# Kernel optimization log

Hardware: AMD Instinct MI355X
Metric: run time of the kernel (lower is better)

Reference implementation:

```python
import jax, jax.numpy as jnp
import numpy as np

N_NODES = 100000
N_EDGES = 3200000
DIMS = [3, 64, 64, 64, 128, 1024, 512, 256, 2]  # per GCNemb.__init__


def setup_inputs() -> dict:
    key = jax.random.key(0)
    ks = jax.random.split(key, 2 + 2 * 8)
    x = jax.random.normal(ks[0], (N_NODES, DIMS[0]), dtype=jnp.float32)
    edge_index = jax.random.randint(ks[1], (2, N_EDGES), 0, N_NODES, dtype=jnp.int64)
    inp = {"x": x, "edge_index": edge_index}
    for i in range(8):
        scale = 1.0 / np.sqrt(DIMS[i])
        inp[f"W{i}"] = jax.random.normal(ks[2 + 2 * i], (DIMS[i], DIMS[i + 1]), dtype=jnp.float32) * scale
        inp[f"b{i}"] = jnp.zeros((DIMS[i + 1],), dtype=jnp.float32)
    return inp


def _gcn_norm(edge_index, n):
    # PyG GCNConv default: add self-loops, symmetric normalization.
    loop = jnp.arange(n, dtype=edge_index.dtype)
    row = jnp.concatenate([edge_index[0], loop])  # source
    col = jnp.concatenate([edge_index[1], loop])  # target
    deg = jax.ops.segment_sum(jnp.ones_like(col, dtype=jnp.float32), col, num_segments=n)
    dinv = jnp.where(deg > 0, jax.lax.rsqrt(deg), 0.0)
    norm = dinv[row] * dinv[col]  # [E+N]
    return row, col, norm


def _gcn_conv(x, W, b, row, col, norm, n):
    h = x @ W  # [N, out]
    agg = jax.ops.segment_sum(h[row] * norm[:, None], col, num_segments=n)
    return agg + b


def reference(x, edge_index, W0, b0, W1, b1, W2, b2, W3, b3, W4, b4, W5, b5, W6, b6, W7, b7):
    n = x.shape[0]
    row, col, norm = _gcn_norm(edge_index, n)
    Ws = [W0, W1, W2, W3, W4, W5, W6, W7]
    bs = [b0, b1, b2, b3, b4, b5, b6, b7]
    for i in range(7):
        x = jax.nn.relu(_gcn_conv(x, Ws[i], bs[i], row, col, norm, n))
    return _gcn_conv(x, Ws[7], bs[7], row, col, norm, n)
```

## Files before the change

### kernel.cpp

```cpp
#include <hip/hip_runtime.h>
#include <hip/hip_bf16.h>
#include <cstdint>
#include <cstddef>


#define TPB 256

typedef short short8 __attribute__((ext_vector_type(8)));
typedef float f32x4 __attribute__((ext_vector_type(4)));

__device__ __forceinline__ float b2f(unsigned short u) {
    union { unsigned int i; float f; } c; c.i = ((unsigned int)u) << 16; return c.f;
}
__device__ __forceinline__ unsigned short f2b(float f) {
    __hip_bfloat16 h = __float2bfloat16(f);
    union { __hip_bfloat16 h; unsigned short u; } c; c.h = h; return c.u;
}

__device__ __forceinline__ void async_copy16(void* lds, const void* g) {
    __builtin_amdgcn_global_load_lds(
        (const __attribute__((address_space(1))) void*)g,
        (__attribute__((address_space(3))) void*)lds,
        16, 0, 0);
}


__global__ void count_deg_kernel(const int* __restrict__ col, int* __restrict__ deg,
                                 int E, int n) {
    int e = blockIdx.x * blockDim.x + threadIdx.x;
    if (e < E) {
        int c = col[e];
        if ((unsigned)c < (unsigned)n) atomicAdd(&deg[c], 1);
    }
}

__global__ void dinv_kernel(const int* __restrict__ deg, float* __restrict__ dinv, int n) {
    int i = blockIdx.x * blockDim.x + threadIdx.x;
    if (i < n) dinv[i] = 1.0f / sqrtf((float)(deg[i] + 1));
}

__global__ void scan_kernel(const int* __restrict__ deg, int* __restrict__ rowptr,
                            int* __restrict__ cursor, int n) {
    __shared__ int sums[1024];
    int tid = threadIdx.x;
    int chunk = (n + 1023) >> 10;
    int lo = tid * chunk;
    int hi = lo + chunk; if (hi > n) hi = n;
    int s = 0;
    for (int i = lo; i < hi; i++) s += deg[i];
    sums[tid] = s;
    __syncthreads();
    for (int off = 1; off < 1024; off <<= 1) {
        int v = (tid >= off) ? sums[tid - off] : 0;
        __syncthreads();
        sums[tid] += v;
        __syncthreads();
    }
    int run = (tid == 0) ? 0 : sums[tid - 1];
    for (int i = lo; i < hi; i++) {
        rowptr[i] = run; cursor[i] = run;
        run += deg[i];
    }
    if (tid == 1023) rowptr[n] = sums[1023];
}

__global__ void fill_csr_kernel(const int* __restrict__ row, const int* __restrict__ col,
                                const float* __restrict__ dinv,
                                int* __restrict__ cursor, int2* __restrict__ es,
                                int E, int n) {
    int e = blockIdx.x * blockDim.x + threadIdx.x;
    if (e < E) {
        int c = col[e];
        if ((unsigned)c < (unsigned)n) {
            int r = row[e];
            int pos = atomicAdd(&cursor[c], 1);
            if ((unsigned)pos < (unsigned)E) {
                es[pos] = make_int2(r, __float_as_int(dinv[r]));
            }
        }
    }
}

__global__ void convert_wt_kernel(const float* __restrict__ W, unsigned short* __restrict__ Wt,
                                  int K, int M) {
    int idx = blockIdx.x * blockDim.x + threadIdx.x;
    if (idx < K * M) {
        int k = idx / M, m = idx % M;
        Wt[(size_t)m * K + k] = f2b(W[idx]);
    }
}


template <int VEC> struct Pack;
template <> struct Pack<1> { using T = unsigned short; };
template <> struct Pack<2> { using T = unsigned int; };
template <> struct Pack<4> { using T = uint2; };

template <int VEC>
__global__ __launch_bounds__(TPB) void agg_win_kernel(
        const unsigned short* __restrict__ x, unsigned short* __restrict__ out,
        const int* __restrict__ rowptr, const int2* __restrict__ es,
        const float* __restrict__ dinv, const float* __restrict__ bias,
        int n, int d, int wb, int relu) {
    using P = typename Pack<VEC>::T;
    int wid  = (blockIdx.x * blockDim.x + threadIdx.x) >> 6;
    int lane = threadIdx.x & 63;
    if (wid >= n) return;
    int start = rowptr[wid], end = rowptr[wid + 1];
    float acc0[VEC], acc1[VEC], acc2[VEC], acc3[VEC];
#pragma unroll
    for (int j = 0; j < VEC; j++) { acc0[j] = 0.f; acc1[j] = 0.f; acc2[j] = 0.f; acc3[j] = 0.f; }
    const int fo = wb + lane * VEC;
    union U { P v; unsigned short u[VEC]; };

    for (int base = start; base < end; base += 64) {
        int idx = base + lane;
        int clamped = (idx < end) ? idx : (end - 1);
        int2 ev = es[clamped];
        int   sv = ev.x;
        float dv = (idx < end) ? __int_as_float(ev.y) : 0.f;
        int cnt = end - base; if (cnt > 64) cnt = 64;
        int j = 0;
        for (; j + 4 <= cnt; j += 4) {
            int   s0 = __shfl(sv, j),     s1 = __shfl(sv, j + 1);
            int   s2 = __shfl(sv, j + 2), s3 = __shfl(sv, j + 3);
            float e0 = __shfl(dv, j),     e1 = __shfl(dv, j + 1);
            float e2 = __shfl(dv, j + 2), e3 = __shfl(dv, j + 3);
            U l0, l1, l2, l3;
            l0.v = *(const P*)(x + (size_t)s0 * d + fo);
            l1.v = *(const P*)(x + (size_t)s1 * d + fo);
            l2.v = *(const P*)(x + (size_t)s2 * d + fo);
            l3.v = *(const P*)(x + (size_t)s3 * d + fo);
#pragma unroll
            for (int q = 0; q < VEC; q++) {
                acc0[q] = fmaf(e0, b2f(l0.u[q]), acc0[q]);
                acc1[q] = fmaf(e1, b2f(l1.u[q]), acc1[q]);
                acc2[q] = fmaf(e2, b2f(l2.u[q]), acc2[q]);
                acc3[q] = fmaf(e3, b2f(l3.u[q]), acc3[q]);
            }
        }
        for (; j < cnt; j++) {
            int   s0 = __shfl(sv, j);
            float e0 = __shfl(dv, j);
            U l0; l0.v = *(const P*)(x + (size_t)s0 * d + fo);
#pragma unroll
            for (int q = 0; q < VEC; q++) acc0[q] = fmaf(e0, b2f(l0.u[q]), acc0[q]);
        }
    }

    float di = dinv[wid];
    U ls; ls.v = *(const P*)(x + (size_t)wid * d + fo);
    U st;
#pragma unroll
    for (int j = 0; j < VEC; j++) {
        float a = (acc0[j] + acc1[j]) + (acc2[j] + acc3[j]);
        float v = di * (a + di * b2f(ls.u[j]));
        if (bias) v += bias[fo + j];
        if (relu) v = fmaxf(v, 0.f);
        st.u[j] = f2b(v);
    }
    *(P*)(out + (size_t)wid * d + fo) = st.v;
}

template <int D, int FUSE64>
__global__ __launch_bounds__(TPB) void agg_small_wave_kernel(
        const float* __restrict__ x, float* __restrict__ outf,
        unsigned short* __restrict__ outb,
        const int* __restrict__ rowptr, const int2* __restrict__ es,
        const float* __restrict__ dinv, const float* __restrict__ bias,
        const float* __restrict__ W, int n, int relu) {
    int wid  = (blockIdx.x * blockDim.x + threadIdx.x) >> 6;
    int lane = threadIdx.x & 63;
    if (wid >= n) return;
    int start = rowptr[wid], end = rowptr[wid + 1];
    float acc[D];
#pragma unroll
    for (int j = 0; j < D; j++) acc[j] = 0.f;
    for (int e = start + lane; e < end; e += 64) {
        int2 ev = es[e];
        int s = ev.x;
        float ds = __int_as_float(ev.y);
#pragma unroll
        for (int j = 0; j < D; j++) acc[j] = fmaf(ds, x[(size_t)s * D + j], acc[j]);
    }
#pragma unroll
    for (int j = 0; j < D; j++) {
#pragma unroll
        for (int off = 32; off >= 1; off >>= 1) acc[j] += __shfl_xor(acc[j], off);
    }
    float di = dinv[wid];
    float aggv[D];
#pragma unroll
    for (int j = 0; j < D; j++) aggv[j] = di * (acc[j] + di * x[(size_t)wid * D + j]);

    if (FUSE64) {
        float v = bias[lane];
#pragma unroll
        for (int j = 0; j < D; j++) v = fmaf(aggv[j], W[j * 64 + lane], v);
        v = fmaxf(v, 0.f);
        outb[(size_t)wid * 64 + lane] = f2b(v);
    } else {
        if (lane < D) {
            float v = aggv[lane];
            if (bias) v += bias[lane];
            if (relu) v = fmaxf(v, 0.f);
            outf[(size_t)wid * D + lane] = v;
        }
    }
}

__global__ __launch_bounds__(TPB) void gemm_dot2_kernel(
        const unsigned short* __restrict__ A, const float* __restrict__ W,
        float* __restrict__ pre, int n) {
    int wid  = (blockIdx.x * blockDim.x + threadIdx.x) >> 6;
    int lane = threadIdx.x & 63;
    if (wid >= n) return;
    union { uint2 v; unsigned short u[4]; } a;
    a.v = *(const uint2*)(A + (size_t)wid * 256 + lane * 4);
    float c0 = 0.f, c1 = 0.f;
#pragma unroll
    for (int j = 0; j < 4; j++) {
        float av = b2f(a.u[j]);
        c0 = fmaf(av, W[(lane * 4 + j) * 2 + 0], c0);
        c1 = fmaf(av, W[(lane * 4 + j) * 2 + 1], c1);
    }
#pragma unroll
    for (int off = 32; off >= 1; off >>= 1) {
        c0 += __shfl_xor(c0, off);
        c1 += __shfl_xor(c1, off);
    }
    if (lane == 0) { pre[(size_t)wid * 2 + 0] = c0; pre[(size_t)wid * 2 + 1] = c1; }
}

__device__ inline float to_f(float v) { return v; }
__device__ inline float to_f(__hip_bfloat16 v) { return __bfloat162float(v); }
__device__ inline void from_f(float v, float& d) { d = v; }
__device__ inline void from_f(float v, __hip_bfloat16& d) { d = __float2bfloat16(v); }

#define BM 64
#define BN 64
#define BK 16
template <typename TA, typename TC>
__global__ __launch_bounds__(256) void gemm_valu_kernel(
        const TA* __restrict__ A, const float* __restrict__ W,
        const float* __restrict__ bias, TC* __restrict__ C,
        int nr, int K, int M, int relu, int addbias) {
    __shared__ float As[BK][BM + 4];
    __shared__ float Bs[BK][BN + 4];
    int tid  = threadIdx.x;
    int row0 = blockIdx.x * BM;
    int col0 = blockIdx.y * BN;
    int rm = (tid >> 4) << 2;
    int rn = (tid & 15) << 2;
    float acc[4][4];
#pragma unroll
    for (int y = 0; y < 4; y++)
#pragma unroll
        for (int xj = 0; xj < 4; xj++) acc[y][xj] = 0.f;

    for (int kk = 0; kk < K; kk += BK) {
#pragma unroll
        for (int i = 0; i < 4; i++) {
            int idx = tid + i * 256;
            int k = idx & 15, r = idx >> 4;
            int gr = row0 + r, gk = kk + k;
            float v = 0.f;
            if (gr < nr && gk < K) v = to_f(A[(size_t)gr * K + gk]);
            As[k][r] = v;
        }
#pragma unroll
        for (int i = 0; i < 4; i++) {
            int idx = tid + i * 256;
            int k = idx >> 6, c = idx & 63;
            int gk = kk + k, gc = col0 + c;
            float v = 0.f;
            if (gk < K && gc < M) v = W[(size_t)gk * M + gc];
            Bs[k][c] = v;
        }
        __syncthreads();
#pragma unroll
        for (int k = 0; k < BK; k++) {
            float a[4], b[4];
#pragma unroll
            for (int j = 0; j < 4; j++) { a[j] = As[k][rm + j]; b[j] = Bs[k][rn + j]; }
#pragma unroll
            for (int y = 0; y < 4; y++)
#pragma unroll
                for (int xj = 0; xj < 4; xj++)
                    acc[y][xj] = fmaf(a[y], b[xj], acc[y][xj]);
        }
        __syncthreads();
    }
#pragma unroll
    for (int y = 0; y < 4; y++) {
        int gr = row0 + rm + y;
        if (gr >= nr) continue;
#pragma unroll
        for (int xj = 0; xj < 4; xj++) {
            int gc = col0 + rn + xj;
            if (gc >= M) continue;
            float v = acc[y][xj];
            if (addbias) v += bias[gc];
            if (relu) v = fmaxf(v, 0.f);
            from_f(v, C[(size_t)gr * M + gc]);
        }
    }
}

template <typename TA, typename TC>
static inline void launch_gemm_valu(const TA* A, const float* W, const float* bias,
                                    TC* C, int nr, int K, int M, int relu, int addbias,
                                    hipStream_t stream) {
    dim3 grid((nr + BM - 1) / BM, (M + BN - 1) / BN);
    gemm_valu_kernel<TA, TC><<<grid, 256, 0, stream>>>(A, W, bias, C, nr, K, M, relu, addbias);
}

__global__ __launch_bounds__(256) void gemm_mfma_kernel(
        const unsigned short* __restrict__ A, const unsigned short* __restrict__ Wt,
        const float* __restrict__ bias, unsigned short* __restrict__ C,
        int nr, int K, int M, int relu, int addbias) {
    __shared__ alignas(16) short As[128 * 32];
    __shared__ alignas(16) short Bs[128 * 32];
    const int tid  = threadIdx.x;
    const int w    = tid >> 6;
    const int lane = tid & 63;
    const int wr   = w >> 1;
    const int wc   = w & 1;
    const int row0 = blockIdx.x * 128;
    const int col0 = blockIdx.y * 128;

    f32x4 acc[4][4];
#pragma unroll
    for (int i = 0; i < 4; i++)
#pragma unroll
        for (int j = 0; j < 4; j++) acc[i][j] = {0.f, 0.f, 0.f, 0.f};

    const int lrow   = lane >> 2;
    const int lcolB  = (lane & 3) * 16;
    const int fm     = lane & 15;
    const int fq     = lane >> 4;

    for (int kk = 0; kk < K; kk += 32) {
#pragma unroll
        for (int i = 0; i < 2; i++) {
            int r = w * 32 + i * 16 + lrow;
            int grow = row0 + r;
            const char* g = (const char*)A + ((size_t)grow * K + kk) * 2 + lcolB;
            short* lds = &As[(w * 32 + i * 16) * 32];
            if (grow < nr) async_copy16(lds, g);
        }
#pragma unroll
        for (int i = 0; i < 2; i++) {
            int r = w * 32 + i * 16 + lrow;
            int gcol = col0 + r;
            const char* g = (const char*)Wt + ((size_t)gcol * K + kk) * 2 + lcolB;
            short* lds = &Bs[(w * 32 + i * 16) * 32];
            async_copy16(lds, g);
        }
        __syncthreads();

        short8 a[4], b[4];
#pragma unroll
        for (int i = 0; i < 4; i++) {
            a[i] = *(const short8*)&As[(wr * 64 + i * 16 + fm) * 32 + fq * 8];
            b[i] = *(const short8*)&Bs[(wc * 64 + i * 16 + fm) * 32 + fq * 8];
        }
#pragma unroll
        for (int mi = 0; mi < 4; mi++)
#pragma unroll
            for (int ni = 0; ni < 4; ni++)
                acc[mi][ni] = __builtin_amdgcn_mfma_f32_16x16x32_bf16(
                    a[mi], b[ni], acc[mi][ni], 0, 0, 0);
        __syncthreads();
    }

#pragma unroll
    for (int mi = 0; mi < 4; mi++) {
#pragma unroll
        for (int r = 0; r < 4; r++) {
            int row = row0 + wr * 64 + mi * 16 + fq * 4 + r;
            if (row >= nr) continue;
            size_t rb = (size_t)row * M;
#pragma unroll
            for (int ni = 0; ni < 4; ni++) {
                int col = col0 + wc * 64 + ni * 16 + fm;
                float v = acc[mi][ni][r];
                if (addbias) v += bias[col];
                if (relu) v = fmaxf(v, 0.f);
                C[rb + col] = f2b(v);
            }
        }
    }
}

static inline void launch_gemm_mfma(const unsigned short* A, const unsigned short* Wt,
                                    const float* bias, unsigned short* C,
                                    int nr, int K, int M, int relu, int addbias,
                                    hipStream_t stream) {
    dim3 grid((nr + 127) / 128, M / 128);
    gemm_mfma_kernel<<<grid, 256, 0, stream>>>(A, Wt, bias, C, nr, K, M, relu, addbias);
}


static inline size_t al256(size_t x) { return (x + 255) & ~(size_t)255; }

extern "C" void kernel_launch(void* const* d_in, const int* in_sizes, int n_in,
                              void* d_out, int out_size, void* d_ws, size_t ws_size,
                              hipStream_t stream) {
    const float* x  = (const float*)d_in[0];
    const int*   ei = (const int*)d_in[1];
    const int E = in_sizes[1] / 2;
    const int n = in_sizes[0] / 3;
    const int* rowv = ei;
    const int* colv = ei + E;

    const float* Wf[8]; const float* bt[8];
    for (int i = 0; i < 8; i++) { Wf[i] = (const float*)d_in[2 + 2 * i]; bt[i] = (const float*)d_in[3 + 2 * i]; }

    char* p = (char*)d_ws;
    size_t used = 0;
    auto carve = [&](size_t bytes) -> char* {
        char* r = p + used; used += al256(bytes); return r;
    };
    int*   deg    = (int*)carve((size_t)n * 4);
    float* dinv   = (float*)carve((size_t)n * 4);
    int*   rowptr = (int*)carve((size_t)(n + 1) * 4);
    int*   cursor = (int*)carve((size_t)(n + 1) * 4);
    int2*  es     = (int2*)carve((size_t)E * 8);
    unsigned short* bufA = (unsigned short*)carve((size_t)n * 512 * 2);
    unsigned short* bufB = (unsigned short*)carve((size_t)n * 512 * 2);
    const size_t wt3e = 64 * 128, wt4e = 128 * 1024, wt5e = 1024 * 512, wt6e = 512 * 256;
    unsigned short* wt3 = (unsigned short*)carve((wt3e + wt4e + wt5e + wt6e) * 2);
    unsigned short* wt4 = wt3 + wt3e;
    unsigned short* wt5 = wt4 + wt4e;
    unsigned short* wt6 = wt5 + wt5e;
    size_t avail = (ws_size > used) ? (ws_size - used) : 0;
    int chunk = (int)(avail / (1024 * 2));
    if (chunk > n) chunk = n;
    chunk &= ~127;
    if (chunk < 2048) chunk = 2048;
    char* tmp_raw = carve((size_t)chunk * 1024 * 2);
    unsigned short* tmpb = (unsigned short*)tmp_raw;
    float* tmpf = (float*)tmp_raw;

    const int EB = (E + TPB - 1) / TPB;
    const int NB = (n + TPB - 1) / TPB;
    const int NW = (n + 3) / 4;

    hipMemsetAsync(deg, 0, (size_t)n * 4, stream);
    count_deg_kernel<<<EB, TPB, 0, stream>>>(colv, deg, E, n);
    dinv_kernel<<<NB, TPB, 0, stream>>>(deg, dinv, n);
    scan_kernel<<<1, 1024, 0, stream>>>(deg, rowptr, cursor, n);
    fill_csr_kernel<<<EB, TPB, 0, stream>>>(rowv, colv, dinv, cursor, es, E, n);

    convert_wt_kernel<<<(int)((wt3e + 255) / 256), 256, 0, stream>>>(Wf[3], wt3, 64, 128);
    convert_wt_kernel<<<(int)((wt4e + 255) / 256), 256, 0, stream>>>(Wf[4], wt4, 128, 1024);
    convert_wt_kernel<<<(int)((wt5e + 255) / 256), 256, 0, stream>>>(Wf[5], wt5, 1024, 512);
    convert_wt_kernel<<<(int)((wt6e + 255) / 256), 256, 0, stream>>>(Wf[6], wt6, 512, 256);

    agg_small_wave_kernel<3, 1><<<NW, TPB, 0, stream>>>(
        x, nullptr, bufA, rowptr, es, dinv, bt[0], Wf[0], n, 1);

    agg_win_kernel<1><<<NW, TPB, 0, stream>>>(bufA, bufB, rowptr, es, dinv, nullptr, n, 64, 0, 0);
    launch_gemm_valu<__hip_bfloat16, __hip_bfloat16>((const __hip_bfloat16*)bufB, Wf[1], bt[1],
                                                     (__hip_bfloat16*)bufA, n, 64, 64, 1, 1, stream);
    agg_win_kernel<1><<<NW, TPB, 0, stream>>>(bufA, bufB, rowptr, es, dinv, nullptr, n, 64, 0, 0);
    launch_gemm_valu<__hip_bfloat16, __hip_bfloat16>((const __hip_bfloat16*)bufB, Wf[2], bt[2],
                                                     (__hip_bfloat16*)bufA, n, 64, 64, 1, 1, stream);

    agg_win_kernel<1><<<NW, TPB, 0, stream>>>(bufA, bufB, rowptr, es, dinv, nullptr, n, 64, 0, 0);
    launch_gemm_mfma(bufB, wt3, bt[3], bufA, n, 64, 128, 1, 1, stream);

    agg_win_kernel<2><<<NW, TPB, 0, stream>>>(bufA, bufB, rowptr, es, dinv, nullptr, n, 128, 0, 0);
    for (int r0 = 0; r0 < n; r0 += chunk) {
        int ch = n - r0; if (ch > chunk) ch = chunk;
        launch_gemm_mfma(bufB + (size_t)r0 * 128, wt4, bt[4], tmpb, ch, 128, 1024, 1, 1, stream);
        launch_gemm_mfma(tmpb, wt5, nullptr, bufA + (size_t)r0 * 512, ch, 1024, 512, 0, 0, stream);
    }
    agg_win_kernel<4><<<NW, TPB, 0, stream>>>(bufA, bufB, rowptr, es, dinv, bt[5], n, 512, 0, 1);
    agg_win_kernel<4><<<NW, TPB, 0, stream>>>(bufA, bufB, rowptr, es, dinv, bt[5], n, 512, 256, 1);

    launch_gemm_mfma(bufB, wt6, nullptr, bufA, n, 512, 256, 0, 0, stream);
    agg_win_kernel<4><<<NW, TPB, 0, stream>>>(bufA, bufB, rowptr, es, dinv, bt[6], n, 256, 0, 1);

    gemm_dot2_kernel<<<NW, TPB, 0, stream>>>(bufB, Wf[7], tmpf, n);
    agg_small_wave_kernel<2, 0><<<NW, TPB, 0, stream>>>(
        tmpf, (float*)d_out, nullptr, rowptr, es, dinv, bt[7], nullptr, n, 0);
}
```

Baseline: 2.221 ms.

## Fuse 64-wide aggregation with GEMM and parallelize the CSR prefix scan

Replaces the single-block serial scan with a three-pass block-parallel scan (block sums, scan of the sums, local scan plus write). Layers 1 and 2 now use one kernel per layer: it aggregates neighbours, then multiplies by a 64x64 weight held in shared memory and applies bias and ReLU. This removes two intermediate activation round trips and two VALU GEMM launches. In exchange, each block reloads the 16KB weight into LDS, and the per-lane 64-step dot product adds LDS traffic.

```diff
diff --git a/kernel.cpp b/kernel.cpp
--- a/kernel.cpp
+++ b/kernel.cpp
@@ -5,6 +5,8 @@
 
 
 #define TPB 256
+#define SI 8
+#define STILE (TPB * SI)
 
 typedef short short8 __attribute__((ext_vector_type(8)));
 typedef float f32x4 __attribute__((ext_vector_type(4)));
@@ -39,29 +41,69 @@
     if (i < n) dinv[i] = 1.0f / sqrtf((float)(deg[i] + 1));
 }
 
-__global__ void scan_kernel(const int* __restrict__ deg, int* __restrict__ rowptr,
-                            int* __restrict__ cursor, int n) {
+__global__ __launch_bounds__(TPB) void scan_part1(const int* __restrict__ deg,
+                                                  int* __restrict__ bsum, int n) {
+    int t0 = blockIdx.x * STILE + threadIdx.x * SI;
+    int s = 0;
+#pragma unroll
+    for (int j = 0; j < SI; j++) { int i = t0 + j; if (i < n) s += deg[i]; }
+#pragma unroll
+    for (int off = 32; off >= 1; off >>= 1) s += __shfl_xor(s, off);
+    __shared__ int ws[TPB / 64];
+    if ((threadIdx.x & 63) == 0) ws[threadIdx.x >> 6] = s;
+    __syncthreads();
+    if (threadIdx.x == 0) {
+        int tot = 0;
+        for (int i = 0; i < TPB / 64; i++) tot += ws[i];
+        bsum[blockIdx.x] = tot;
+    }
+}
+
+__global__ void scan_part2(int* __restrict__ bsum, int nb,
+                           int* __restrict__ rowptr, int n) {
     __shared__ int sums[1024];
     int tid = threadIdx.x;
-    int chunk = (n + 1023) >> 10;
-    int lo = tid * chunk;
-    int hi = lo + chunk; if (hi > n) hi = n;
-    int s = 0;
-    for (int i = lo; i < hi; i++) s += deg[i];
-    sums[tid] = s;
+    int v = (tid < nb) ? bsum[tid] : 0;
+    sums[tid] = v;
     __syncthreads();
     for (int off = 1; off < 1024; off <<= 1) {
-        int v = (tid >= off) ? sums[tid - off] : 0;
+        int t = (tid >= off) ? sums[tid - off] : 0;
         __syncthreads();
-        sums[tid] += v;
+        sums[tid] += t;
         __syncthreads();
     }
-    int run = (tid == 0) ? 0 : sums[tid - 1];
-    for (int i = lo; i < hi; i++) {
-        rowptr[i] = run; cursor[i] = run;
-        run += deg[i];
-    }
-    if (tid == 1023) rowptr[n] = sums[1023];
+    if (tid < nb) bsum[tid] = (tid == 0) ? 0 : sums[tid - 1];
+    if (tid == 0) rowptr[n] = sums[1023];
+}
+
+__global__ __launch_bounds__(TPB) void scan_part3(const int* __restrict__ deg,
+                                                  const int* __restrict__ bsum,
+                                                  int* __restrict__ rowptr,
+                                                  int* __restrict__ cursor, int n) {
+    int tid = threadIdx.x;
+    int lane = tid & 63, wv = tid >> 6;
+    int t0 = blockIdx.x * STILE + tid * SI;
+    int v[SI]; int s = 0;
+#pragma unroll
+    for (int j = 0; j < SI; j++) { int i = t0 + j; v[j] = (i < n) ? deg[i] : 0; s += v[j]; }
+    int sc = s;
+#pragma unroll
+    for (int off = 1; off < 64; off <<= 1) {
+        int t = __shfl_up(sc, off);
+        if (lane >= off) sc += t;
+    }
+    __shared__ int wtot[TPB / 64];
+    if (lane == 63) wtot[wv] = sc;
+    __syncthreads();
+    int woff = 0;
+    for (int i = 0; i < wv; i++) woff += wtot[i];
+    int off0 = bsum[blockIdx.x] + woff + (sc - s);
+#pragma unroll
+    for (int j = 0; j < SI; j++) {
+        int i = t0 + j;
+        if (i < n) { rowptr[i] = off0; cursor[i] = off0; }
+        off0 += v[j];
+    }
 }
 
 __global__ void fill_csr_kernel(const int* __restrict__ row, const int* __restrict__ col,
@@ -162,6 +204,56 @@
     *(P*)(out + (size_t)wid * d + fo) = st.v;
 }
 
+__global__ __launch_bounds__(TPB) void agg_gemm64_kernel(
+        const unsigned short* __restrict__ x, unsigned short* __restrict__ out,
+        const int* __restrict__ rowptr, const int2* __restrict__ es,
+        const float* __restrict__ dinv, const float* __restrict__ W,
+        const float* __restrict__ bias, int n) {
+    __shared__ float Ws[64 * 64];
+    __shared__ float aggs[TPB / 64][64];
+    const int tid = threadIdx.x;
+    for (int i = tid; i < 64 * 64; i += TPB) Ws[i] = W[i];
+    __syncthreads();
+    int wid  = (blockIdx.x * TPB + tid) >> 6;
+    int lane = tid & 63;
+    int wv   = tid >> 6;
+    if (wid >= n) return;
+    int start = rowptr[wid], end = rowptr[wid + 1];
+    float acc0 = 0.f, acc1 = 0.f, acc2 = 0.f, acc3 = 0.f;
+    for (int base = start; base < end; base += 64) {
+        int idx = base + lane;
+        int clamped = (idx < end) ? idx : (end - 1);
+        int2 ev = es[clamped];
+        int   sv = ev.x;
+        float dv = (idx < end) ? __int_as_float(ev.y) : 0.f;
+        int cnt = end - base; if (cnt > 64) cnt = 64;
+        int j = 0;
+        for (; j + 4 <= cnt; j += 4) {
+            int   s0 = __shfl(sv, j),     s1 = __shfl(sv, j + 1);
+            int   s2 = __shfl(sv, j + 2), s3 = __shfl(sv, j + 3);
+            float e0 = __shfl(dv, j),     e1 = __shfl(dv, j + 1);
+            float e2 = __shfl(dv, j + 2), e3 = __shfl(dv, j + 3);
+            acc0 = fmaf(e0, b2f(x[(size_t)s0 * 64 + lane]), acc0);
+            acc1 = fmaf(e1, b2f(x[(size_t)s1 * 64 + lane]), acc1);
+            acc2 = fmaf(e2, b2f(x[(size_t)s2 * 64 + lane]), acc2);
+            acc3 = fmaf(e3, b2f(x[(size_t)s3 * 64 + lane]), acc3);
+        }
+        for (; j < cnt; j++) {
+            int   s0 = __shfl(sv, j);
+            float e0 = __shfl(dv, j);
+            acc0 = fmaf(e0, b2f(x[(size_t)s0 * 64 + lane]), acc0);
+        }
+    }
+    float di = dinv[wid];
+    float a = di * (((acc0 + acc1) + (acc2 + acc3)) + di * b2f(x[(size_t)wid * 64 + lane]));
+    aggs[wv][lane] = a;
+    float v = bias[lane];
+#pragma unroll 8
+    for (int j = 0; j < 64; j++) v = fmaf(aggs[wv][j], Ws[j * 64 + lane], v);
+    v = fmaxf(v, 0.f);
+    out[(size_t)wid * 64 + lane] = f2b(v);
+}
+
 template <int D, int FUSE64>
 __global__ __launch_bounds__(TPB) void agg_small_wave_kernel(
         const float* __restrict__ x, float* __restrict__ outf,
@@ -230,89 +322,6 @@
         c1 += __shfl_xor(c1, off);
     }
     if (lane == 0) { pre[(size_t)wid * 2 + 0] = c0; pre[(size_t)wid * 2 + 1] = c1; }
-}
-
-__device__ inline float to_f(float v) { return v; }
-__device__ inline float to_f(__hip_bfloat16 v) { return __bfloat162float(v); }
-__device__ inline void from_f(float v, float& d) { d = v; }
-__device__ inline void from_f(float v, __hip_bfloat16& d) { d = __float2bfloat16(v); }
-
-#define BM 64
-#define BN 64
-#define BK 16
-template <typename TA, typename TC>
-__global__ __launch_bounds__(256) void gemm_valu_kernel(
-        const TA* __restrict__ A, const float* __restrict__ W,
-        const float* __restrict__ bias, TC* __restrict__ C,
-        int nr, int K, int M, int relu, int addbias) {
-    __shared__ float As[BK][BM + 4];
-    __shared__ float Bs[BK][BN + 4];
-    int tid  = threadIdx.x;
-    int row0 = blockIdx.x * BM;
-    int col0 = blockIdx.y * BN;
-    int rm = (tid >> 4) << 2;
-    int rn = (tid & 15) << 2;
-    float acc[4][4];
-#pragma unroll
-    for (int y = 0; y < 4; y++)
-#pragma unroll
-        for (int xj = 0; xj < 4; xj++) acc[y][xj] = 0.f;
-
-    for (int kk = 0; kk < K; kk += BK) {
-#pragma unroll
-        for (int i = 0; i < 4; i++) {
-            int idx = tid + i * 256;
-            int k = idx & 15, r = idx >> 4;
-            int gr = row0 + r, gk = kk + k;
-            float v = 0.f;
-            if (gr < nr && gk < K) v = to_f(A[(size_t)gr * K + gk]);
-            As[k][r] = v;
-        }
-#pragma unroll
-        for (int i = 0; i < 4; i++) {
-            int idx = tid + i * 256;
-            int k = idx >> 6, c = idx & 63;
-            int gk = kk + k, gc = col0 + c;
-            float v = 0.f;
-            if (gk < K && gc < M) v = W[(size_t)gk * M + gc];
-            Bs[k][c] = v;
-        }
-        __syncthreads();
-#pragma unroll
-        for (int k = 0; k < BK; k++) {
-            float a[4], b[4];
-#pragma unroll
-            for (int j = 0; j < 4; j++) { a[j] = As[k][rm + j]; b[j] = Bs[k][rn + j]; }
-#pragma unroll
-            for (int y = 0; y < 4; y++)
-#pragma unroll
-                for (int xj = 0; xj < 4; xj++)
-                    acc[y][xj] = fmaf(a[y], b[xj], acc[y][xj]);
-        }
-        __syncthreads();
-    }
-#pragma unroll
-    for (int y = 0; y < 4; y++) {
-        int gr = row0 + rm + y;
-        if (gr >= nr) continue;
-#pragma unroll
-        for (int xj = 0; xj < 4; xj++) {
-            int gc = col0 + rn + xj;
-            if (gc >= M) continue;
-            float v = acc[y][xj];
-            if (addbias) v += bias[gc];
-            if (relu) v = fmaxf(v, 0.f);
-            from_f(v, C[(size_t)gr * M + gc]);
-        }
-    }
-}
-
-template <typename TA, typename TC>
-static inline void launch_gemm_valu(const TA* A, const float* W, const float* bias,
-                                    TC* C, int nr, int K, int M, int relu, int addbias,
-                                    hipStream_t stream) {
-    dim3 grid((nr + BM - 1) / BM, (M + BN - 1) / BN);
-    gemm_valu_kernel<TA, TC><<<grid, 256, 0, stream>>>(A, W, bias, C, nr, K, M, relu, addbias);
 }
 
 __global__ __launch_bounds__(256) void gemm_mfma_kernel(
@@ -426,6 +435,7 @@
     float* dinv   = (float*)carve((size_t)n * 4);
     int*   rowptr = (int*)carve((size_t)(n + 1) * 4);
     int*   cursor = (int*)carve((size_t)(n + 1) * 4);
+    int*   bsum   = (int*)carve(4096 * 4);
     int2*  es     = (int2*)carve((size_t)E * 8);
     unsigned short* bufA = (unsigned short*)carve((size_t)n * 512 * 2);
     unsigned short* bufB = (unsigned short*)carve((size_t)n * 512 * 2);
@@ -446,11 +456,14 @@
     const int EB = (E + TPB - 1) / TPB;
     const int NB = (n + TPB - 1) / TPB;
     const int NW = (n + 3) / 4;
+    const int SBK = (n + STILE - 1) / STILE;
 
     hipMemsetAsync(deg, 0, (size_t)n * 4, stream);
     count_deg_kernel<<<EB, TPB, 0, stream>>>(colv, deg, E, n);
     dinv_kernel<<<NB, TPB, 0, stream>>>(deg, dinv, n);
-    scan_kernel<<<1, 1024, 0, stream>>>(deg, rowptr, cursor, n);
+    scan_part1<<<SBK, TPB, 0, stream>>>(deg, bsum, n);
+    scan_part2<<<1, 1024, 0, stream>>>(bsum, SBK, rowptr, n);
+    scan_part3<<<SBK, TPB, 0, stream>>>(deg, bsum, rowptr, cursor, n);
     fill_csr_kernel<<<EB, TPB, 0, stream>>>(rowv, colv, dinv, cursor, es, E, n);
 
     convert_wt_kernel<<<(int)((wt3e + 255) / 256), 256, 0, stream>>>(Wf[3], wt3, 64, 128);
@@ -461,12 +474,8 @@
     agg_small_wave_kernel<3, 1><<<NW, TPB, 0, stream>>>(
         x, nullptr, bufA, rowptr, es, dinv, bt[0], Wf[0], n, 1);
 
-    agg_win_kernel<1><<<NW, TPB, 0, stream>>>(bufA, bufB, rowptr, es, dinv, nullptr, n, 64, 0, 0);
-    launch_gemm_valu<__hip_bfloat16, __hip_bfloat16>((const __hip_bfloat16*)bufB, Wf[1], bt[1],
-                                                     (__hip_bfloat16*)bufA, n, 64, 64, 1, 1, stream);
-    agg_win_kernel<1><<<NW, TPB, 0, stream>>>(bufA, bufB, rowptr, es, dinv, nullptr, n, 64, 0, 0);
-    launch_gemm_valu<__hip_bfloat16, __hip_bfloat16>((const __hip_bfloat16*)bufB, Wf[2], bt[2],
-                                                     (__hip_bfloat16*)bufA, n, 64, 64, 1, 1, stream);
+    agg_gemm64_kernel<<<NW, TPB, 0, stream>>>(bufA, bufB, rowptr, es, dinv, Wf[1], bt[1], n);
+    agg_gemm64_kernel<<<NW, TPB, 0, stream>>>(bufB, bufA, rowptr, es, dinv, Wf[2], bt[2], n);
 
     agg_win_kernel<1><<<NW, TPB, 0, stream>>>(bufA, bufB, rowptr, es, dinv, nullptr, n, 64, 0, 0);
     launch_gemm_mfma(bufB, wt3, bt[3], bufA, n, 64, 128, 1, 1, stream);
```

After: 2.036 ms. 8.3% less time.
